# Performance work log

Measured on AMD Instinct MI355X. Metric: run time of the kernel, lower is better.

## Reference

```python
import jax, jax.numpy as jnp
import numpy as np

N_NODES = 100000


def gcn_conv(x, edge_index, W, b):
    # GCNConv with add_self_loops=True, normalize=True (symmetric norm):
    # out = D^{-1/2} (A + I) D^{-1/2} (x @ W) + b
    n = x.shape[0]
    h = x @ W  # transform first (PyG applies lin before propagate)
    src, dst = edge_index[0], edge_index[1]
    ones = jnp.ones(src.shape[0], dtype=h.dtype)
    # degree with self-loops: in-degree + 1
    deg = jax.ops.segment_sum(ones, dst, num_segments=n) + 1.0
    dinv = jax.lax.rsqrt(deg)  # deg >= 1, always finite
    # per-edge normalized messages, scatter-add to dst
    msg = h[src] * (dinv[src] * dinv[dst])[:, None]
    agg = jax.ops.segment_sum(msg, dst, num_segments=n)
    # self-loop contribution: norm = dinv[i]^2
    agg = agg + h * (dinv * dinv)[:, None]
    return agg + b


def setup_inputs() -> dict:
    key = jax.random.key(0)
    ks = jax.random.split(key, 8)
    x = jax.random.normal(ks[0], (N_NODES, 256), dtype=jnp.float32)
    edge_index = jax.random.randint(ks[1], (2, 3200000), 0, N_NODES, dtype=jnp.int32)
    W1 = jax.random.normal(ks[2], (256, 32), dtype=jnp.float32) * (1.0 / np.sqrt(256))
    b1 = jnp.zeros((32,), dtype=jnp.float32)
    Wm = jax.random.normal(ks[3], (32, 16), dtype=jnp.float32) * (1.0 / np.sqrt(32))
    bm = jnp.zeros((16,), dtype=jnp.float32)
    Wv = jax.random.normal(ks[4], (32, 16), dtype=jnp.float32) * (1.0 / np.sqrt(32))
    bv = jnp.zeros((16,), dtype=jnp.float32)
    return {"x": x, "edge_index": edge_index, "W1": W1, "b1": b1,
            "Wm": Wm, "bm": bm, "Wv": Wv, "bv": bv}


def reference(x, edge_index, W1, b1, Wm, bm, Wv, bv):
    h = jax.nn.relu(gcn_conv(x, edge_index, W1, b1))
    mu = gcn_conv(h, edge_index, Wm, bm)
    sigma = gcn_conv(h, edge_index, Wv, bv)
    return (mu, sigma)
```

## Files before the change

### kernel.cpp

```cpp
#include <hip/hip_runtime.h>
#include <hip/hip_fp16.h>

#define NNODES 100000
#define NEDGES 3200000
#define F_IN   256
#define F_HID  32
#define F_OUT  16

#define NB   196
#define NPB  512
#define CAP  20480
#define NCHUNK 256
#define CHUNK  12500
#define RPT_B  20
#define RPT_A  13

#define GRID1 ((NNODES + 63) / 64)

typedef _Float16 half_t;
typedef half_t half8 __attribute__((ext_vector_type(8)));
typedef float f32x4 __attribute__((ext_vector_type(4)));


__global__ void k_init(int* __restrict__ bcur) {
    if (threadIdx.x < NB) bcur[threadIdx.x] = threadIdx.x * CAP;
}

__global__ __launch_bounds__(1024) void k_phaseA(
        const int* __restrict__ src, const int* __restrict__ dst,
        int* __restrict__ bcur, unsigned int* __restrict__ rec) {
    __shared__ int lh[NB];
    __shared__ int lcur[NB];
    int t = threadIdx.x;
    int e0 = blockIdx.x * CHUNK;
    if (t < NB) lh[t] = 0;

    int dcache[RPT_A];
    #pragma unroll
    for (int k = 0; k < RPT_A; ++k) {
        int i = t + k * 1024;
        dcache[k] = (i < CHUNK) ? dst[e0 + i] : -1;
    }
    __syncthreads();
    #pragma unroll
    for (int k = 0; k < RPT_A; ++k)
        if (dcache[k] >= 0) atomicAdd(&lh[dcache[k] >> 9], 1);
    __syncthreads();
    if (t < NB) lcur[t] = lh[t] ? atomicAdd(&bcur[t], lh[t]) : 0;
    __syncthreads();
    #pragma unroll
    for (int k = 0; k < RPT_A; ++k) {
        int i = t + k * 1024;
        if (dcache[k] >= 0) {
            int s = src[e0 + i];
            int d = dcache[k];
            int b = d >> 9;
            int pos = atomicAdd(&lcur[b], 1);
            rec[pos] = ((unsigned)s << 9) | (unsigned)(d & 511);
        }
    }
}

__global__ __launch_bounds__(1024) void k_phaseB(
        const unsigned int* __restrict__ rec, const int* __restrict__ bcur,
        int* __restrict__ rowptr, int* __restrict__ cnt,
        float* __restrict__ dinv, int* __restrict__ csr) {
    __shared__ int lh[NPB];
    __shared__ int lsc[NPB];
    __shared__ int wsum[16];
    int t = threadIdx.x, b = blockIdx.x;
    int lo = b * CAP;
    int nrec = bcur[b] - lo;
    if (t < NPB) lh[t] = 0;

    unsigned rcache[RPT_B];
    #pragma unroll
    for (int k = 0; k < RPT_B; ++k) {
        int i = t + k * 1024;
        rcache[k] = (i < nrec) ? rec[lo + i] : 0xFFFFFFFFu;
    }
    __syncthreads();
    #pragma unroll
    for (int k = 0; k < RPT_B; ++k)
        if (rcache[k] != 0xFFFFFFFFu) atomicAdd(&lh[rcache[k] & 511], 1);
    __syncthreads();

    int lane = t & 63, w = t >> 6;
    int my = (t < NPB) ? lh[t] : 0;
    int v = my;
    #pragma unroll
    for (int d = 1; d < 64; d <<= 1) {
        int tmp = __shfl_up(v, d, 64);
        if (lane >= d) v += tmp;
    }
    if (lane == 63) wsum[w] = v;
    __syncthreads();
    if (w == 0) {
        int s = (lane < 16) ? wsum[lane] : 0;
        #pragma unroll
        for (int d = 1; d < 16; d <<= 1) {
            int tmp = __shfl_up(s, d, 64);
            if (lane >= d) s += tmp;
        }
        if (lane < 16) wsum[lane] = s;
    }
    __syncthreads();
    int ex = v + (w > 0 ? wsum[w - 1] : 0) - my;
    int node = b * NPB + t;
    if (t < NPB) {
        lsc[t] = ex;
        if (node < NNODES) {
            rowptr[node] = lo + ex;
            cnt[node] = my;
            dinv[node] = rsqrtf((float)my + 1.0f);
        }
    }
    __syncthreads();
    #pragma unroll
    for (int k = 0; k < RPT_B; ++k)
        if (rcache[k] != 0xFFFFFFFFu) {
            int dl = rcache[k] & 511;
            int p = atomicAdd(&lsc[dl], 1);
            csr[lo + p] = (int)(rcache[k] >> 9);
        }
}


__global__ __launch_bounds__(256) void k_gemm1(
        const float* __restrict__ x, const float* __restrict__ W1,
        const float* __restrict__ dinv, __half2* __restrict__ g1) {
    __shared__ half_t Wt[32 * 264];
    __shared__ float sb4[4][16 * 33];
    int t = threadIdx.x;
    int wave = t >> 6, lane = t & 63;
    int m = lane & 15, q = lane >> 4;
    int row0 = blockIdx.x * 64 + wave * 16;

    for (int i = t; i < F_IN * F_HID; i += 256) {
        int k = i >> 5, f = i & 31;
        Wt[f * 264 + k] = (half_t)W1[i];
    }
    __syncthreads();

    half8 B[2][8];
    #pragma unroll
    for (int ft = 0; ft < 2; ++ft)
        #pragma unroll
        for (int kc = 0; kc < 8; ++kc)
            B[ft][kc] = *(const half8*)&Wt[(ft * 16 + m) * 264 + kc * 32 + q * 8];

    int grow_a = row0 + m; if (grow_a >= NNODES) grow_a = NNODES - 1;
    const float* rowp = &x[(size_t)grow_a * F_IN + q * 8];

    f32x4 acc0 = {0.f, 0.f, 0.f, 0.f};
    f32x4 acc1 = {0.f, 0.f, 0.f, 0.f};
    #pragma unroll
    for (int kb = 0; kb < 8; ++kb) {
        const float* sp = rowp + kb * 32;
        float4 xa = *(const float4*)sp;
        float4 xb = *(const float4*)(sp + 4);
        half8 A;
        A[0] = (half_t)xa.x; A[1] = (half_t)xa.y;
        A[2] = (half_t)xa.z; A[3] = (half_t)xa.w;
        A[4] = (half_t)xb.x; A[5] = (half_t)xb.y;
        A[6] = (half_t)xb.z; A[7] = (half_t)xb.w;
        acc0 = __builtin_amdgcn_mfma_f32_16x16x32_f16(A, B[0][kb], acc0, 0, 0, 0);
        acc1 = __builtin_amdgcn_mfma_f32_16x16x32_f16(A, B[1][kb], acc1, 0, 0, 0);
    }

    float* sb = sb4[wave];
    #pragma unroll
    for (int r = 0; r < 4; ++r) {
        int rl = q * 4 + r;
        int grow = row0 + rl; if (grow >= NNODES) grow = NNODES - 1;
        float dv = dinv[grow];
        sb[rl * 33 + m]      = acc0[r] * dv;
        sb[rl * 33 + 16 + m] = acc1[r] * dv;
    }
    __syncthreads();
    int rl = (t >> 2) & 15;
    int w2 = t >> 6;
    int c0 = (t & 3) * 8;
    int grow = blockIdx.x * 64 + w2 * 16 + rl;
    if (grow < NNODES) {
        const float* sp = &sb4[w2][rl * 33 + c0];
        __half2 h0 = __floats2half2_rn(sp[0], sp[1]);
        __half2 h1 = __floats2half2_rn(sp[2], sp[3]);
        __half2 h2 = __floats2half2_rn(sp[4], sp[5]);
        __half2 h3 = __floats2half2_rn(sp[6], sp[7]);
        __half2* gp = &g1[(size_t)grow * 16 + (c0 >> 1)];
        gp[0] = h0; gp[1] = h1; gp[2] = h2; gp[3] = h3;
    }
}


__global__ __launch_bounds__(256) void k_gather_l1(
        const int* __restrict__ rowptr, const int* __restrict__ cnt,
        const int* __restrict__ csr,
        const float* __restrict__ dinv, const __half2* __restrict__ g,
        const float* __restrict__ b1, const float* __restrict__ Wm,
        const float* __restrict__ Wv, __half2* __restrict__ g2) {
    __shared__ float Wcat[F_HID * 32];
    __shared__ float hrow[16][F_HID + 2];
    int tx = threadIdx.x;
    for (int idx = tx; idx < F_HID * 32; idx += 256) {
        int k = idx >> 5, j = idx & 31;
        Wcat[idx] = (j < F_OUT) ? Wm[k * F_OUT + j] : Wv[k * F_OUT + (j - F_OUT)];
    }
    int f2 = tx & 15;
    int lr = tx >> 4;
    int node = blockIdx.x * 16 + lr;
    int start = rowptr[node], end = start + cnt[node];
    float2 acc = __half22float2(g[(size_t)node * 16 + f2]);
    int j = start;
    for (; j + 8 <= end; j += 8) {
        int s[8];
        #pragma unroll
        for (int u = 0; u < 8; ++u) s[u] = csr[j + u];
        float2 a[8];
        #pragma unroll
        for (int u = 0; u < 8; ++u) a[u] = __half22float2(g[(size_t)s[u] * 16 + f2]);
        float sx = 0.f, sy = 0.f;
        #pragma unroll
        for (int u = 0; u < 8; ++u) { sx += a[u].x; sy += a[u].y; }
        acc.x += sx; acc.y += sy;
    }
    for (; j + 4 <= end; j += 4) {
        int s0 = csr[j], s1 = csr[j + 1], s2 = csr[j + 2], s3 = csr[j + 3];
        float2 a0 = __half22float2(g[(size_t)s0 * 16 + f2]);
        float2 a1 = __half22float2(g[(size_t)s1 * 16 + f2]);
        float2 a2 = __half22float2(g[(size_t)s2 * 16 + f2]);
        float2 a3 = __half22float2(g[(size_t)s3 * 16 + f2]);
        acc.x += (a0.x + a1.x) + (a2.x + a3.x);
        acc.y += (a0.y + a1.y) + (a2.y + a3.y);
    }
    for (; j < end; ++j) {
        float2 a = __half22float2(g[(size_t)csr[j] * 16 + f2]);
        acc.x += a.x; acc.y += a.y;
    }
    float dv = dinv[node];
    float h0 = dv * acc.x + b1[2 * f2];
    float h1 = dv * acc.y + b1[2 * f2 + 1];
    hrow[lr][2 * f2]     = h0 > 0.f ? h0 : 0.f;
    hrow[lr][2 * f2 + 1] = h1 > 0.f ? h1 : 0.f;
    __syncthreads();
    float o0 = 0.f, o1 = 0.f;
    #pragma unroll
    for (int k = 0; k < F_HID; ++k) {
        float hv = hrow[lr][k];
        o0 = fmaf(hv, Wcat[k * 32 + 2 * f2], o0);
        o1 = fmaf(hv, Wcat[k * 32 + 2 * f2 + 1], o1);
    }
    g2[(size_t)node * 16 + f2] = __floats2half2_rn(o0 * dv, o1 * dv);
}


__global__ __launch_bounds__(256) void k_gather_out(
        const int* __restrict__ rowptr, const int* __restrict__ cnt,
        const int* __restrict__ csr,
        const float* __restrict__ dinv, const __half2* __restrict__ g,
        const float* __restrict__ bm, const float* __restrict__ bv,
        float* __restrict__ out) {
    int tx = threadIdx.x;
    int f2 = tx & 15;
    int node = blockIdx.x * 16 + (tx >> 4);
    int start = rowptr[node], end = start + cnt[node];
    float2 acc = __half22float2(g[(size_t)node * 16 + f2]);
    int j = start;
    for (; j + 8 <= end; j += 8) {
        int s[8];
        #pragma unroll
        for (int u = 0; u < 8; ++u) s[u] = csr[j + u];
        float2 a[8];
        #pragma unroll
        for (int u = 0; u < 8; ++u) a[u] = __half22float2(g[(size_t)s[u] * 16 + f2]);
        float sx = 0.f, sy = 0.f;
        #pragma unroll
        for (int u = 0; u < 8; ++u) { sx += a[u].x; sy += a[u].y; }
        acc.x += sx; acc.y += sy;
    }
    for (; j + 4 <= end; j += 4) {
        int s0 = csr[j], s1 = csr[j + 1], s2 = csr[j + 2], s3 = csr[j + 3];
        float2 a0 = __half22float2(g[(size_t)s0 * 16 + f2]);
        float2 a1 = __half22float2(g[(size_t)s1 * 16 + f2]);
        float2 a2 = __half22float2(g[(size_t)s2 * 16 + f2]);
        float2 a3 = __half22float2(g[(size_t)s3 * 16 + f2]);
        acc.x += (a0.x + a1.x) + (a2.x + a3.x);
        acc.y += (a0.y + a1.y) + (a2.y + a3.y);
    }
    for (; j < end; ++j) {
        float2 a = __half22float2(g[(size_t)csr[j] * 16 + f2]);
        acc.x += a.x; acc.y += a.y;
    }
    float dv = dinv[node];
    int f = 2 * f2;
    if (f < F_OUT) {
        float2 o = { dv * acc.x + bm[f], dv * acc.y + bm[f + 1] };
        *(float2*)&out[(size_t)node * F_OUT + f] = o;
    } else {
        float2 o = { dv * acc.x + bv[f - F_OUT], dv * acc.y + bv[f - F_OUT + 1] };
        *(float2*)&out[(size_t)NNODES * F_OUT + (size_t)node * F_OUT + (f - F_OUT)] = o;
    }
}


extern "C" void kernel_launch(void* const* d_in, const int* in_sizes, int n_in,
                              void* d_out, int out_size, void* d_ws, size_t ws_size,
                              hipStream_t stream) {
    const float* x   = (const float*)d_in[0];
    const int*   ei  = (const int*)  d_in[1];
    const float* W1  = (const float*)d_in[2];
    const float* b1  = (const float*)d_in[3];
    const float* Wm  = (const float*)d_in[4];
    const float* bm  = (const float*)d_in[5];
    const float* Wv  = (const float*)d_in[6];
    const float* bv  = (const float*)d_in[7];
    float* out = (float*)d_out;

    const int* src = ei;
    const int* dst = ei + NEDGES;

    char* ws = (char*)d_ws;
    float*        dinv   = (float*)ws;        ws += 100352 * 4;
    int*          bcur   = (int*)ws;          ws += 256 * 4;
    int*          rowptr = (int*)ws;          ws += 100352 * 4;
    int*          cnt    = (int*)ws;          ws += 100352 * 4;
    int*          csr    = (int*)ws;          ws += (size_t)NB * CAP * 4;
    unsigned int* rec    = (unsigned int*)ws; ws += (size_t)NB * CAP * 4;
    __half2*      g2     = (__half2*)ws;

    __half2* g1 = (__half2*)rec;

    k_init  <<<1, 256, 0, stream>>>(bcur);
    k_phaseA<<<NCHUNK, 1024, 0, stream>>>(src, dst, bcur, rec);
    k_phaseB<<<NB, 1024, 0, stream>>>(rec, bcur, rowptr, cnt, dinv, csr);

    k_gemm1<<<GRID1, 256, 0, stream>>>(x, W1, dinv, g1);

    k_gather_l1<<<NNODES / 16, 256, 0, stream>>>(rowptr, cnt, csr, dinv, g1, b1, Wm, Wv, g2);

    k_gather_out<<<NNODES / 16, 256, 0, stream>>>(rowptr, cnt, csr, dinv, g2, bm, bv, out);
}
```

Baseline: 320.7 us.

## Co-schedule layer-1 GEMM with edge bucketing in one launch, defer dinv scaling

The first GEMM (x·W1) now runs in the same launch as the edge-bucketing phase A. The block index picks which job a block does, so the bandwidth-heavy read of x can overlap with the atomic-heavy edge scatter. Because dinv is not ready until phase B finishes, the GEMM writes an unscaled fp32 intermediate. A new small kernel then applies the dinv scaling and converts to half. The trade-off is an extra fp32 buffer write and read, plus one more launch, and it needs more workspace.

Measured after the change: 324.1 us. No clear change (+1.1%).

```diff
diff --git a/kernel.cpp b/kernel.cpp
--- a/kernel.cpp
+++ b/kernel.cpp
@@ -15,7 +15,7 @@
 #define RPT_B  20
 #define RPT_A  13
 
-#define GRID1 ((NNODES + 63) / 64)
+#define GRID1B ((NNODES + 255) / 256)
 
 typedef _Float16 half_t;
 typedef half_t half8 __attribute__((ext_vector_type(8)));
@@ -26,37 +26,102 @@
     if (threadIdx.x < NB) bcur[threadIdx.x] = threadIdx.x * CAP;
 }
 
-__global__ __launch_bounds__(1024) void k_phaseA(
+
+__global__ __launch_bounds__(1024) void k_fused(
         const int* __restrict__ src, const int* __restrict__ dst,
-        int* __restrict__ bcur, unsigned int* __restrict__ rec) {
-    __shared__ int lh[NB];
-    __shared__ int lcur[NB];
+        int* __restrict__ bcur, unsigned int* __restrict__ rec,
+        const float* __restrict__ x, const float* __restrict__ W1,
+        float* __restrict__ g1f) {
+    __shared__ union {
+        struct { int lh[NB]; int lcur[NB]; } pa;
+        struct { half_t Wt[32 * 264]; float sbf[16][16 * 33]; } gm;
+    } u;
     int t = threadIdx.x;
-    int e0 = blockIdx.x * CHUNK;
-    if (t < NB) lh[t] = 0;
-
-    int dcache[RPT_A];
-    #pragma unroll
-    for (int k = 0; k < RPT_A; ++k) {
-        int i = t + k * 1024;
-        dcache[k] = (i < CHUNK) ? dst[e0 + i] : -1;
-    }
-    __syncthreads();
-    #pragma unroll
-    for (int k = 0; k < RPT_A; ++k)
-        if (dcache[k] >= 0) atomicAdd(&lh[dcache[k] >> 9], 1);
-    __syncthreads();
-    if (t < NB) lcur[t] = lh[t] ? atomicAdd(&bcur[t], lh[t]) : 0;
-    __syncthreads();
-    #pragma unroll
-    for (int k = 0; k < RPT_A; ++k) {
-        int i = t + k * 1024;
-        if (dcache[k] >= 0) {
-            int s = src[e0 + i];
-            int d = dcache[k];
-            int b = d >> 9;
-            int pos = atomicAdd(&lcur[b], 1);
-            rec[pos] = ((unsigned)s << 9) | (unsigned)(d & 511);
+
+    if (blockIdx.x < NCHUNK) {
+        int e0 = blockIdx.x * CHUNK;
+        if (t < NB) u.pa.lh[t] = 0;
+
+        int dcache[RPT_A];
+        #pragma unroll
+        for (int k = 0; k < RPT_A; ++k) {
+            int i = t + k * 1024;
+            dcache[k] = (i < CHUNK) ? dst[e0 + i] : -1;
+        }
+        __syncthreads();
+        #pragma unroll
+        for (int k = 0; k < RPT_A; ++k)
+            if (dcache[k] >= 0) atomicAdd(&u.pa.lh[dcache[k] >> 9], 1);
+        __syncthreads();
+        if (t < NB) u.pa.lcur[t] = u.pa.lh[t] ? atomicAdd(&bcur[t], u.pa.lh[t]) : 0;
+        __syncthreads();
+        #pragma unroll
+        for (int k = 0; k < RPT_A; ++k) {
+            int i = t + k * 1024;
+            if (dcache[k] >= 0) {
+                int s = src[e0 + i];
+                int d = dcache[k];
+                int b = d >> 9;
+                int pos = atomicAdd(&u.pa.lcur[b], 1);
+                rec[pos] = ((unsigned)s << 9) | (unsigned)(d & 511);
+            }
+        }
+    } else {
+        int gb = blockIdx.x - NCHUNK;
+        int wave = t >> 6, lane = t & 63;
+        int m = lane & 15, q = lane >> 4;
+        int row0 = gb * 256 + wave * 16;
+
+        for (int i = t; i < F_IN * F_HID; i += 1024) {
+            int k = i >> 5, f = i & 31;
+            u.gm.Wt[f * 264 + k] = (half_t)W1[i];
+        }
+        __syncthreads();
+
+        half8 B[2][8];
+        #pragma unroll
+        for (int ft = 0; ft < 2; ++ft)
+            #pragma unroll
+            for (int kc = 0; kc < 8; ++kc)
+                B[ft][kc] = *(const half8*)&u.gm.Wt[(ft * 16 + m) * 264 + kc * 32 + q * 8];
+
+        int grow_a = row0 + m; if (grow_a >= NNODES) grow_a = NNODES - 1;
+        const float* rowp = &x[(size_t)grow_a * F_IN + q * 8];
+
+        f32x4 acc0 = {0.f, 0.f, 0.f, 0.f};
+        f32x4 acc1 = {0.f, 0.f, 0.f, 0.f};
+        #pragma unroll
+        for (int kb = 0; kb < 8; ++kb) {
+            const float* sp = rowp + kb * 32;
+            float4 xa = *(const float4*)sp;
+            float4 xb = *(const float4*)(sp + 4);
+            half8 A;
+            A[0] = (half_t)xa.x; A[1] = (half_t)xa.y;
+            A[2] = (half_t)xa.z; A[3] = (half_t)xa.w;
+            A[4] = (half_t)xb.x; A[5] = (half_t)xb.y;
+            A[6] = (half_t)xb.z; A[7] = (half_t)xb.w;
+            acc0 = __builtin_amdgcn_mfma_f32_16x16x32_f16(A, B[0][kb], acc0, 0, 0, 0);
+            acc1 = __builtin_amdgcn_mfma_f32_16x16x32_f16(A, B[1][kb], acc1, 0, 0, 0);
+        }
+
+        float* sb = u.gm.sbf[wave];
+        #pragma unroll
+        for (int r = 0; r < 4; ++r) {
+            int rl = q * 4 + r;
+            sb[rl * 33 + m]      = acc0[r];
+            sb[rl * 33 + 16 + m] = acc1[r];
+        }
+        __syncthreads();
+        int rl = (t >> 2) & 15;
+        int w2 = t >> 6;
+        int c0 = (t & 3) * 8;
+        int grow = gb * 256 + w2 * 16 + rl;
+        if (grow < NNODES) {
+            const float* sp = &u.gm.sbf[w2][rl * 33 + c0];
+            float4 o0 = { sp[0], sp[1], sp[2], sp[3] };
+            float4 o1 = { sp[4], sp[5], sp[6], sp[7] };
+            float4* gp = (float4*)&g1f[(size_t)grow * 32 + c0];
+            gp[0] = o0; gp[1] = o1;
         }
     }
 }
@@ -126,71 +191,18 @@
 }
 
 
-__global__ __launch_bounds__(256) void k_gemm1(
-        const float* __restrict__ x, const float* __restrict__ W1,
-        const float* __restrict__ dinv, __half2* __restrict__ g1) {
-    __shared__ half_t Wt[32 * 264];
-    __shared__ float sb4[4][16 * 33];
-    int t = threadIdx.x;
-    int wave = t >> 6, lane = t & 63;
-    int m = lane & 15, q = lane >> 4;
-    int row0 = blockIdx.x * 64 + wave * 16;
-
-    for (int i = t; i < F_IN * F_HID; i += 256) {
-        int k = i >> 5, f = i & 31;
-        Wt[f * 264 + k] = (half_t)W1[i];
-    }
-    __syncthreads();
-
-    half8 B[2][8];
-    #pragma unroll
-    for (int ft = 0; ft < 2; ++ft)
-        #pragma unroll
-        for (int kc = 0; kc < 8; ++kc)
-            B[ft][kc] = *(const half8*)&Wt[(ft * 16 + m) * 264 + kc * 32 + q * 8];
-
-    int grow_a = row0 + m; if (grow_a >= NNODES) grow_a = NNODES - 1;
-    const float* rowp = &x[(size_t)grow_a * F_IN + q * 8];
-
-    f32x4 acc0 = {0.f, 0.f, 0.f, 0.f};
-    f32x4 acc1 = {0.f, 0.f, 0.f, 0.f};
-    #pragma unroll
-    for (int kb = 0; kb < 8; ++kb) {
-        const float* sp = rowp + kb * 32;
-        float4 xa = *(const float4*)sp;
-        float4 xb = *(const float4*)(sp + 4);
-        half8 A;
-        A[0] = (half_t)xa.x; A[1] = (half_t)xa.y;
-        A[2] = (half_t)xa.z; A[3] = (half_t)xa.w;
-        A[4] = (half_t)xb.x; A[5] = (half_t)xb.y;
-        A[6] = (half_t)xb.z; A[7] = (half_t)xb.w;
-        acc0 = __builtin_amdgcn_mfma_f32_16x16x32_f16(A, B[0][kb], acc0, 0, 0, 0);
-        acc1 = __builtin_amdgcn_mfma_f32_16x16x32_f16(A, B[1][kb], acc1, 0, 0, 0);
-    }
-
-    float* sb = sb4[wave];
-    #pragma unroll
-    for (int r = 0; r < 4; ++r) {
-        int rl = q * 4 + r;
-        int grow = row0 + rl; if (grow >= NNODES) grow = NNODES - 1;
-        float dv = dinv[grow];
-        sb[rl * 33 + m]      = acc0[r] * dv;
-        sb[rl * 33 + 16 + m] = acc1[r] * dv;
-    }
-    __syncthreads();
-    int rl = (t >> 2) & 15;
-    int w2 = t >> 6;
-    int c0 = (t & 3) * 8;
-    int grow = blockIdx.x * 64 + w2 * 16 + rl;
-    if (grow < NNODES) {
-        const float* sp = &sb4[w2][rl * 33 + c0];
-        __half2 h0 = __floats2half2_rn(sp[0], sp[1]);
-        __half2 h1 = __floats2half2_rn(sp[2], sp[3]);
-        __half2 h2 = __floats2half2_rn(sp[4], sp[5]);
-        __half2 h3 = __floats2half2_rn(sp[6], sp[7]);
-        __half2* gp = &g1[(size_t)grow * 16 + (c0 >> 1)];
-        gp[0] = h0; gp[1] = h1; gp[2] = h2; gp[3] = h3;
-    }
+__global__ __launch_bounds__(256) void k_scale(
+        const float* __restrict__ g1f, const float* __restrict__ dinv,
+        __half2* __restrict__ g1) {
+    int gid = blockIdx.x * 256 + threadIdx.x;
+    if (gid >= NNODES * 8) return;
+    int row = gid >> 3;
+    float dv = dinv[row];
+    float4 v = ((const float4*)g1f)[gid];
+    __half2 h0 = __floats2half2_rn(v.x * dv, v.y * dv);
+    __half2 h1 = __floats2half2_rn(v.z * dv, v.w * dv);
+    __half2* gp = &g1[(size_t)row * 16 + (gid & 7) * 2];
+    gp[0] = h0; gp[1] = h1;
 }
 
 
@@ -327,15 +339,16 @@
     int*          cnt    = (int*)ws;          ws += 100352 * 4;
     int*          csr    = (int*)ws;          ws += (size_t)NB * CAP * 4;
     unsigned int* rec    = (unsigned int*)ws; ws += (size_t)NB * CAP * 4;
+    float*        g1f    = (float*)ws;        ws += (size_t)100352 * 32 * 4;
     __half2*      g2     = (__half2*)ws;
 
     __half2* g1 = (__half2*)rec;
 
-    k_init  <<<1, 256, 0, stream>>>(bcur);
-    k_phaseA<<<NCHUNK, 1024, 0, stream>>>(src, dst, bcur, rec);
+    k_init <<<1, 256, 0, stream>>>(bcur);
+    k_fused<<<NCHUNK + GRID1B, 1024, 0, stream>>>(src, dst, bcur, rec, x, W1, g1f);
     k_phaseB<<<NB, 1024, 0, stream>>>(rec, bcur, rowptr, cnt, dinv, csr);
 
-    k_gemm1<<<GRID1, 256, 0, stream>>>(x, W1, dinv, g1);
+    k_scale<<<(NNODES * 8 + 255) / 256, 256, 0, stream>>>(g1f, dinv, g1);
 
     k_gather_l1<<<NNODES / 16, 256, 0, stream>>>(rowptr, cnt, csr, dinv, g1, b1, Wm, Wv, g2);
 
```
